# Optimization experiments

Hardware: AMD Instinct MI355X
Metric: run time of the kernel (lower is better)

Reference implementation:

```python
import jax, jax.numpy as jnp
from jax import lax
import numpy as np

DT = 0.02
STEP_JITTER = 0.01
NUM_STEPS = 180
B, H, W, D = 2, 512, 512, 128


def setup_inputs() -> dict:
    key = jax.random.key(0)
    k1, k2, k3 = jax.random.split(key, 3)
    camera_rotation = jnp.tile(jnp.eye(3, dtype=jnp.float32)[None], (B, 1, 1))
    camera_position = jnp.array([[0.0, 0.0, -2.5], [0.3, 0.2, -2.5]], dtype=jnp.float32)
    focal = 300.0 * jnp.ones((B, 2), dtype=jnp.float32)
    principal_point = jnp.full((B, 2), 256.0, dtype=jnp.float32)
    xs = jnp.arange(W, dtype=jnp.float32)
    ys = jnp.arange(H, dtype=jnp.float32)
    gx, gy = jnp.meshgrid(xs, ys, indexing='xy')  # [H,W]
    pixel_coords = jnp.broadcast_to(jnp.stack([gx, gy], -1)[None], (B, H, W, 2))
    template = jax.random.uniform(k1, (B, 4, D, D, D), dtype=jnp.float32)  # RGB + alpha volume
    background = jax.random.uniform(k2, (B, 3, H, W), dtype=jnp.float32)
    return {
        'camera_rotation': camera_rotation, 'camera_position': camera_position,
        'focal': focal, 'principal_point': principal_point,
        'pixel_coords': pixel_coords, 'template': template, 'background': background,
    }


def _trilinear_one(vol, pos):
    # vol [C,D,D,D] indexed [c,z,y,x]; pos [H,W,3] = (x,y,z) in [-1,1]
    Dv = vol.shape[-1]
    g = jnp.clip((pos + 1.0) * 0.5 * (Dv - 1), 0.0, Dv - 1)
    gx, gy, gz = g[..., 0], g[..., 1], g[..., 2]
    x0 = jnp.floor(gx).astype(jnp.int32); x1 = jnp.minimum(x0 + 1, Dv - 1)
    y0 = jnp.floor(gy).astype(jnp.int32); y1 = jnp.minimum(y0 + 1, Dv - 1)
    z0 = jnp.floor(gz).astype(jnp.int32); z1 = jnp.minimum(z0 + 1, Dv - 1)
    wx = (gx - x0)[None]; wy = (gy - y0)[None]; wz = (gz - z0)[None]
    at = lambda z, y, x: vol[:, z, y, x]  # [C,H,W]
    c00 = at(z0, y0, x0) * (1 - wx) + at(z0, y0, x1) * wx
    c01 = at(z0, y1, x0) * (1 - wx) + at(z0, y1, x1) * wx
    c10 = at(z1, y0, x0) * (1 - wx) + at(z1, y0, x1) * wx
    c11 = at(z1, y1, x0) * (1 - wx) + at(z1, y1, x1) * wx
    c0 = c00 * (1 - wy) + c01 * wy
    c1 = c10 * (1 - wy) + c11 * wy
    return c0 * (1 - wz) + c1 * wz  # [C,H,W]


def _march(camera_rotation, camera_position, focal, principal_point, pixel_coords, template, background):
    key = jax.random.key(42)
    rd = (pixel_coords - principal_point[:, None, None, :]) / focal[:, None, None, :]
    rd = jnp.concatenate([rd, jnp.ones_like(rd[..., :1])], axis=-1)
    # torch: sum(R[:,None,None,:,:] * d[...,:,None], dim=-2) == R^T @ d
    rd = jnp.einsum('bjk,bhwj->bhwk', camera_rotation, rd)
    rd = rd / jnp.sqrt(jnp.sum(rd * rd, axis=-1, keepdims=True))
    cp = camera_position[:, None, None, :]
    # ray/box intersection (no_grad in original)
    t1 = (-1.0 - cp) / rd
    t2 = (1.0 - cp) / rd
    t_min = jnp.maximum(jnp.minimum(t1[..., 0], t2[..., 0]),
                        jnp.maximum(jnp.minimum(t1[..., 1], t2[..., 1]),
                                    jnp.minimum(t1[..., 2], t2[..., 2])))
    t_max = jnp.minimum(jnp.maximum(t1[..., 0], t2[..., 0]),
                        jnp.minimum(jnp.maximum(t1[..., 1], t2[..., 1]),
                                    jnp.maximum(t1[..., 2], t2[..., 2])))
    hit = t_min < t_max
    t = jnp.maximum(jnp.where(hit, t_min, 0.0), 0.0)
    t = lax.stop_gradient(t)
    t = t - DT * jax.random.uniform(jax.random.fold_in(key, 0), t.shape, dtype=t.dtype)
    ray_pos = cp + rd * t[..., None]                      # [B,H,W,3]
    ray_rgb = jnp.zeros_like(jnp.moveaxis(ray_pos, -1, 1))  # [B,3,H,W]
    ray_alpha = jnp.zeros_like(ray_rgb[:, :1])             # [B,1,H,W]
    ray_length = jnp.zeros_like(ray_alpha)
    sample = jax.vmap(_trilinear_one)

    def body(carry, i):
        ray_pos, t, ray_rgb, ray_alpha, ray_length = carry
        valid = jnp.all((ray_pos > -1.0) & (ray_pos < 1.0), axis=-1)
        valid_f = valid[:, None].astype(ray_rgb.dtype)      # [B,1,H,W]
        s = sample(template, ray_pos)                       # [B,4,H,W]
        sample_rgb, sample_alpha = s[:, :3], s[:, 3:4]
        noise = jax.random.normal(jax.random.fold_in(key, i + 1), t.shape, dtype=t.dtype)
        step = lax.stop_gradient(DT * jnp.exp(STEP_JITTER * noise))  # [B,H,W]
        contrib = (jnp.minimum(ray_alpha + sample_alpha * step[:, None], 1.0) - ray_alpha) * valid_f
        ray_rgb = ray_rgb + sample_rgb * contrib
        ray_alpha = ray_alpha + contrib
        ray_length = ray_length + step[:, None] * (contrib == 0)
        ray_pos = ray_pos + rd * step[..., None]
        t = t + step
        return (ray_pos, t, ray_rgb, ray_alpha, ray_length), None

    carry = (ray_pos, t, ray_rgb, ray_alpha, ray_length)
    (ray_pos, t, ray_rgb, ray_alpha, ray_length), _ = lax.scan(body, carry, jnp.arange(NUM_STEPS))
    ray_length = ray_alpha * ray_length / (jnp.max(ray_length) + jnp.min(ray_length))
    ray_rgb = ray_rgb + (1.0 - ray_alpha) * jnp.maximum(background, 0.0)
    return ray_rgb, ray_alpha, ray_length


def reference(camera_rotation, camera_position, focal, principal_point, pixel_coords, template, background):
    return _march(camera_rotation, camera_position, focal, principal_point, pixel_coords, template, background)
```

## Files before the change

### kernel.cpp

```cpp
#include <hip/hip_runtime.h>
#include <stdint.h>

#pragma clang fp contract(off)

#define Bn 2
#define Hn 512
#define Wn 512
#define Dn 128
#define HW (Hn * Wn)
#define NRAY (Bn * HW)
#define NSTEP 180
#define DTC 0.02f
#define D3 (Dn * Dn * Dn)

#define WS_AOS_BYTE_OFF 4096
#define WS_AOS_BYTES ((size_t)Bn * D3 * 16)

typedef float f2 __attribute__((ext_vector_type(2)));

#define KEXP  ((float)(0.01 * (double)1.41421354f * 1.4426950408889634))
#define LOG2DT (-5.643856189774724f)

__device__ __forceinline__ uint32_t rotl32(uint32_t x, int n) {
    return (x << n) | (x >> (32 - n));
}

__device__ __forceinline__ void tf2x32(uint32_t k0, uint32_t k1,
                                       uint32_t& x0, uint32_t& x1) {
    uint32_t k2 = k0 ^ k1 ^ 0x1BD11BDAu;
    x0 += k0; x1 += k1;
    x0 += x1; x1 = rotl32(x1, 13); x1 ^= x0;
    x0 += x1; x1 = rotl32(x1, 15); x1 ^= x0;
    x0 += x1; x1 = rotl32(x1, 26); x1 ^= x0;
    x0 += x1; x1 = rotl32(x1, 6);  x1 ^= x0;
    x0 += k1; x1 += k2 + 1u;
    x0 += x1; x1 = rotl32(x1, 17); x1 ^= x0;
    x0 += x1; x1 = rotl32(x1, 29); x1 ^= x0;
    x0 += x1; x1 = rotl32(x1, 16); x1 ^= x0;
    x0 += x1; x1 = rotl32(x1, 24); x1 ^= x0;
    x0 += k2; x1 += k0 + 2u;
    x0 += x1; x1 = rotl32(x1, 13); x1 ^= x0;
    x0 += x1; x1 = rotl32(x1, 15); x1 ^= x0;
    x0 += x1; x1 = rotl32(x1, 26); x1 ^= x0;
    x0 += x1; x1 = rotl32(x1, 6);  x1 ^= x0;
    x0 += k0; x1 += k1 + 3u;
    x0 += x1; x1 = rotl32(x1, 17); x1 ^= x0;
    x0 += x1; x1 = rotl32(x1, 29); x1 ^= x0;
    x0 += x1; x1 = rotl32(x1, 16); x1 ^= x0;
    x0 += x1; x1 = rotl32(x1, 24); x1 ^= x0;
    x0 += k1; x1 += k2 + 4u;
    x0 += x1; x1 = rotl32(x1, 13); x1 ^= x0;
    x0 += x1; x1 = rotl32(x1, 15); x1 ^= x0;
    x0 += x1; x1 = rotl32(x1, 26); x1 ^= x0;
    x0 += x1; x1 = rotl32(x1, 6);  x1 ^= x0;
    x0 += k2; x1 += k0 + 5u;
}

__device__ __forceinline__ uint32_t pbits(uint32_t k0, uint32_t k1, uint32_t i) {
    uint32_t x0 = 0u, x1 = i;
    tf2x32(k0, k1, x0, x1);
    return x0 ^ x1;
}

__device__ __forceinline__ float erfinv_px(float x) {
    float a = x * x;
    float w = -__logf(1.0f - a);
    float p;
    if (w < 5.0f) {
        w = w - 2.5f;
        p = 2.81022636e-08f;
        p = fmaf(p, w, 3.43273939e-07f);
        p = fmaf(p, w, -3.5233877e-06f);
        p = fmaf(p, w, -4.39150654e-06f);
        p = fmaf(p, w, 0.00021858087f);
        p = fmaf(p, w, -0.00125372503f);
        p = fmaf(p, w, -0.00417768164f);
        p = fmaf(p, w, 0.246640727f);
        p = fmaf(p, w, 1.50140941f);
    } else {
        w = sqrtf(w) - 3.0f;
        p = -0.000200214257f;
        p = fmaf(p, w, 0.000100950558f);
        p = fmaf(p, w, 0.00134934322f);
        p = fmaf(p, w, -0.00367342844f);
        p = fmaf(p, w, 0.00573950773f);
        p = fmaf(p, w, -0.0076224613f);
        p = fmaf(p, w, 0.00943887047f);
        p = fmaf(p, w, 1.00167406f);
        p = fmaf(p, w, 2.83297682f);
    }
    return p * x;
}

__device__ __forceinline__ float step_from_bits(uint32_t bits) {
    float uf = __uint_as_float((bits >> 9) | 0x3f800000u);
    float uu = fmaxf(-0.99999994f, fmaf(uf, 2.0f, -3.0f));
    float pw = erfinv_px(uu);
    return __builtin_amdgcn_exp2f(fmaf(pw, KEXP, LOG2DT));
}

__device__ __forceinline__ f2 plerp(f2 a, f2 b, f2 wv) {
    return __builtin_elementwise_fma(wv, b - a, a);
}

__global__ void init_keys_kernel(uint32_t* __restrict__ ws) {
    int t = threadIdx.x;
    if (t <= 180) {
        uint32_t x0 = 0u, x1 = (uint32_t)t;
        tf2x32(0u, 42u, x0, x1);
        ws[2 * t]     = x0;
        ws[2 * t + 1] = x1;
    }
    if (t == 181) ws[362] = 0u;
    if (t == 182) ws[363] = 0x7f7fffffu;
}

__global__ __launch_bounds__(256) void repack_kernel(
    const float* __restrict__ tpl, float4* __restrict__ aos,
    uint32_t* __restrict__ ws) {
    if (blockIdx.x == 0) {
        int t = threadIdx.x;
        if (t <= 180) {
            uint32_t x0 = 0u, x1 = (uint32_t)t;
            tf2x32(0u, 42u, x0, x1);
            ws[2 * t]     = x0;
            ws[2 * t + 1] = x1;
        }
        if (t == 181) ws[362] = 0u;
        if (t == 182) ws[363] = 0x7f7fffffu;
    }
    int i = blockIdx.x * 256 + threadIdx.x;
    if (i >= Bn * D3) return;
    int b = i >> 21;
    int v = i & (D3 - 1);
    const float* base = tpl + (size_t)b * 4 * D3 + v;
    float4 o;
    o.x = base[0];
    o.y = base[D3];
    o.z = base[2 * D3];
    o.w = base[3 * D3];
    aos[i] = o;
}

template <bool PACKED>
__global__ __launch_bounds__(256) void march_kernel(
    const float* __restrict__ rot, const float* __restrict__ cpos,
    const float* __restrict__ focal, const float* __restrict__ pp,
    const float* __restrict__ pix, const float* __restrict__ tpl,
    const float4* __restrict__ aos,
    const float* __restrict__ bg, float* __restrict__ out,
    uint32_t* __restrict__ ws)
{
    #pragma clang fp contract(off)
    __shared__ uint2 skeys[181];
    for (int i = threadIdx.x; i < 181; i += 256) {
        skeys[i] = make_uint2(ws[2 * i], ws[2 * i + 1]);
    }
    __syncthreads();

    const int idx = blockIdx.x * 256 + threadIdx.x;
    const int b = idx >> 18;
    const int p = idx & (HW - 1);

    float px = pix[(size_t)idx * 2 + 0];
    float py = pix[(size_t)idx * 2 + 1];
    float v0 = (px - pp[b * 2 + 0]) / focal[b * 2 + 0];
    float v1 = (py - pp[b * 2 + 1]) / focal[b * 2 + 1];
    const float* R = rot + b * 9;
    float rdx = (R[0] * v0 + R[3] * v1) + R[6];
    float rdy = (R[1] * v0 + R[4] * v1) + R[7];
    float rdz = (R[2] * v0 + R[5] * v1) + R[8];
    float nrm = sqrtf((rdx * rdx + rdy * rdy) + rdz * rdz);
    rdx = rdx / nrm; rdy = rdy / nrm; rdz = rdz / nrm;
    float cpx = cpos[b * 3 + 0], cpy = cpos[b * 3 + 1], cpz = cpos[b * 3 + 2];

    float t1x = (-1.0f - cpx) / rdx, t2x = (1.0f - cpx) / rdx;
    float t1y = (-1.0f - cpy) / rdy, t2y = (1.0f - cpy) / rdy;
    float t1z = (-1.0f - cpz) / rdz, t2z = (1.0f - cpz) / rdz;
    float tmin = fmaxf(fminf(t1x, t2x), fmaxf(fminf(t1y, t2y), fminf(t1z, t2z)));
    float tmax = fminf(fmaxf(t1x, t2x), fminf(fmaxf(t1y, t2y), fmaxf(t1z, t2z)));
    bool hit = tmin < tmax;
    float t = fmaxf(hit ? tmin : 0.0f, 0.0f);

    {
        uint2 k0 = skeys[0];
        uint32_t bits = pbits(k0.x, k0.y, (uint32_t)idx);
        float u = __uint_as_float((bits >> 9) | 0x3f800000u) - 1.0f;
        u = fmaxf(0.0f, u);
        t = t - DTC * u;
    }

    float posx = cpx + rdx * t;
    float posy = cpy + rdy * t;
    float posz = cpz + rdz * t;

    float alpha = 0.0f, len = 0.0f;
    f2 acc_rg = {0.0f, 0.0f};
    float acc_b = 0.0f;
    const float* vol = tpl + (size_t)b * 4 * D3;
    const char* vbase = (const char*)(aos + (size_t)b * D3);
    bool entered = false;

    int i = 0;
    for (; i < NSTEP; ++i) {
        uint2 kk = skeys[i + 1];
        float step = step_from_bits(pbits(kk.x, kk.y, (uint32_t)idx));

        float m = fmaxf(fmaxf(fabsf(posx), fabsf(posy)), fabsf(posz));
        bool valid = m < 1.0f;
        bool sampling = fmaxf(m, alpha) < 1.0f;

        float contrib = 0.0f;
        if (sampling) {
            float gx = fmaf(posx, 63.5f, 63.5f);
            float gy = fmaf(posy, 63.5f, 63.5f);
            float gz = fmaf(posz, 63.5f, 63.5f);
            float fx = floorf(gx), fy = floorf(gy), fz = floorf(gz);
            float wx = gx - fx, wy = gy - fy, wz = gz - fz;
            int ix0 = (int)fx, iy0 = (int)fy, iz0 = (int)fz;

            float sx, sy, sz, sw;
            if (PACKED) {
                uint32_t xb  = (uint32_t)min(ix0, Dn - 2) << 4;
                float wxe = (ix0 < Dn - 1) ? wx : 1.0f;
                uint32_t yb0 = (uint32_t)iy0 << 11;
                uint32_t yb1 = min(yb0 + (1u << 11), (uint32_t)(Dn - 1) << 11);
                uint32_t zb0 = (uint32_t)iz0 << 18;
                uint32_t zb1 = min(zb0 + (1u << 18), (uint32_t)(Dn - 1) << 18);

                uint32_t o00 = zb0 + yb0 + xb;
                uint32_t o01 = zb0 + yb1 + xb;
                uint32_t o10 = zb1 + yb0 + xb;
                uint32_t o11 = zb1 + yb1 + xb;

                float4 A00 = *(const float4*)(vbase + o00);
                float4 B00 = *(const float4*)(vbase + o00 + 16);
                float4 A01 = *(const float4*)(vbase + o01);
                float4 B01 = *(const float4*)(vbase + o01 + 16);
                float4 A10 = *(const float4*)(vbase + o10);
                float4 B10 = *(const float4*)(vbase + o10 + 16);
                float4 A11 = *(const float4*)(vbase + o11);
                float4 B11 = *(const float4*)(vbase + o11 + 16);

                f2 wxv = {wxe, wxe}, wyv = {wy, wy}, wzv = {wz, wz};
                f2 c00rg = plerp((f2){A00.x, A00.y}, (f2){B00.x, B00.y}, wxv);
                f2 c00ba = plerp((f2){A00.z, A00.w}, (f2){B00.z, B00.w}, wxv);
                f2 c01rg = plerp((f2){A01.x, A01.y}, (f2){B01.x, B01.y}, wxv);
                f2 c01ba = plerp((f2){A01.z, A01.w}, (f2){B01.z, B01.w}, wxv);
                f2 c10rg = plerp((f2){A10.x, A10.y}, (f2){B10.x, B10.y}, wxv);
                f2 c10ba = plerp((f2){A10.z, A10.w}, (f2){B10.z, B10.w}, wxv);
                f2 c11rg = plerp((f2){A11.x, A11.y}, (f2){B11.x, B11.y}, wxv);
                f2 c11ba = plerp((f2){A11.z, A11.w}, (f2){B11.z, B11.w}, wxv);
                f2 c0rg = plerp(c00rg, c01rg, wyv);
                f2 c0ba = plerp(c00ba, c01ba, wyv);
                f2 c1rg = plerp(c10rg, c11rg, wyv);
                f2 c1ba = plerp(c10ba, c11ba, wyv);
                f2 srg = plerp(c0rg, c1rg, wzv);
                f2 sba = plerp(c0ba, c1ba, wzv);
                sx = srg.x; sy = srg.y; sz = sba.x; sw = sba.y;
            } else {
                int ix1 = min(ix0 + 1, Dn - 1);
                int iy1 = min(iy0 + 1, Dn - 1);
                int iz1 = min(iz0 + 1, Dn - 1);
                float owx = 1.0f - wx, owy = 1.0f - wy, owz = 1.0f - wz;
                size_t o00 = ((size_t)iz0 * Dn + iy0) * Dn;
                size_t o01 = ((size_t)iz0 * Dn + iy1) * Dn;
                size_t o10 = ((size_t)iz1 * Dn + iy0) * Dn;
                size_t o11 = ((size_t)iz1 * Dn + iy1) * Dn;
                float s[4];
                #pragma unroll
                for (int c = 0; c < 4; ++c) {
                    const float* vc = vol + (size_t)c * D3;
                    float c00 = vc[o00 + ix0] * owx + vc[o00 + ix1] * wx;
                    float c01 = vc[o01 + ix0] * owx + vc[o01 + ix1] * wx;
                    float c10 = vc[o10 + ix0] * owx + vc[o10 + ix1] * wx;
                    float c11 = vc[o11 + ix0] * owx + vc[o11 + ix1] * wx;
                    float cc0 = c00 * owy + c01 * wy;
                    float cc1 = c10 * owy + c11 * wy;
                    s[c] = cc0 * owz + cc1 * wz;
                }
                sx = s[0]; sy = s[1]; sz = s[2]; sw = s[3];
            }
            contrib = fminf(fmaf(sw, step, alpha), 1.0f) - alpha;
            f2 cv = {contrib, contrib};
            acc_rg = __builtin_elementwise_fma((f2){sx, sy}, cv, acc_rg);
            acc_b = fmaf(sz, contrib, acc_b);
        }
        alpha = alpha + contrib;
        if (contrib == 0.0f) len = len + step;
        posx = fmaf(rdx, step, posx);
        posy = fmaf(rdy, step, posy);
        posz = fmaf(rdz, step, posz);

        bool done = (alpha >= 1.0f) || (entered && !valid);
        entered = entered || valid;
        if (__all(done)) { ++i; break; }
    }
    for (; i < NSTEP; ++i) {
        uint2 kk = skeys[i + 1];
        len = len + step_from_bits(pbits(kk.x, kk.y, (uint32_t)idx));
    }

    size_t obase = (size_t)b * 3 * HW + p;
    out[obase]            = acc_rg.x + (1.0f - alpha) * fmaxf(bg[obase], 0.0f);
    out[obase + HW]       = acc_rg.y + (1.0f - alpha) * fmaxf(bg[obase + HW], 0.0f);
    out[obase + 2 * HW]   = acc_b   + (1.0f - alpha) * fmaxf(bg[obase + 2 * HW], 0.0f);
    out[(size_t)Bn * 3 * HW + (size_t)b * HW + p] = alpha;
    out[(size_t)Bn * 4 * HW + (size_t)b * HW + p] = len;

    __shared__ float smax[256];
    __shared__ float smin[256];
    smax[threadIdx.x] = len;
    smin[threadIdx.x] = len;
    __syncthreads();
    for (int s = 128; s > 0; s >>= 1) {
        if (threadIdx.x < s) {
            smax[threadIdx.x] = fmaxf(smax[threadIdx.x], smax[threadIdx.x + s]);
            smin[threadIdx.x] = fminf(smin[threadIdx.x], smin[threadIdx.x + s]);
        }
        __syncthreads();
    }
    if (threadIdx.x == 0) {
        atomicMax((unsigned int*)&ws[362], __float_as_uint(smax[0]));
        atomicMin((unsigned int*)&ws[363], __float_as_uint(smin[0]));
    }
}

__global__ void finalize_kernel(float* __restrict__ out,
                                const uint32_t* __restrict__ ws) {
    #pragma clang fp contract(off)
    int i = blockIdx.x * blockDim.x + threadIdx.x;
    if (i >= NRAY) return;
    float mx = __uint_as_float(ws[362]);
    float mn = __uint_as_float(ws[363]);
    float a = out[(size_t)Bn * 3 * HW + i];
    size_t loff = (size_t)Bn * 4 * HW + i;
    float l = out[loff];
    out[loff] = (a * l) / (mx + mn);
}

extern "C" void kernel_launch(void* const* d_in, const int* in_sizes, int n_in,
                              void* d_out, int out_size, void* d_ws, size_t ws_size,
                              hipStream_t stream) {
    const float* rot   = (const float*)d_in[0];
    const float* cpos  = (const float*)d_in[1];
    const float* focal = (const float*)d_in[2];
    const float* pp    = (const float*)d_in[3];
    const float* pix   = (const float*)d_in[4];
    const float* tpl   = (const float*)d_in[5];
    const float* bg    = (const float*)d_in[6];
    float* out = (float*)d_out;
    uint32_t* ws = (uint32_t*)d_ws;
    float4* aos = (float4*)((char*)d_ws + WS_AOS_BYTE_OFF);

    const bool packed = ws_size >= WS_AOS_BYTE_OFF + WS_AOS_BYTES;

    if (packed) {
        hipLaunchKernelGGL(repack_kernel, dim3((Bn * D3) / 256), dim3(256), 0,
                           stream, tpl, aos, ws);
        hipLaunchKernelGGL(march_kernel<true>, dim3(NRAY / 256), dim3(256), 0,
                           stream, rot, cpos, focal, pp, pix, tpl, aos, bg, out, ws);
    } else {
        hipLaunchKernelGGL(init_keys_kernel, dim3(1), dim3(256), 0, stream, ws);
        hipLaunchKernelGGL(march_kernel<false>, dim3(NRAY / 256), dim3(256), 0,
                           stream, rot, cpos, focal, pp, pix, tpl, aos, bg, out, ws);
    }
    hipLaunchKernelGGL(finalize_kernel, dim3(NRAY / 256), dim3(256), 0, stream,
                       out, ws);
}
```

Baseline: 434.7 us.

## March two rays per thread with interleaved Threefry and per-ray wave masks

```diff
diff --git a/kernel.cpp b/kernel.cpp
--- a/kernel.cpp
+++ b/kernel.cpp
@@ -56,13 +56,36 @@
     x0 += k2; x1 += k0 + 5u;
 }
 
-__device__ __forceinline__ uint32_t pbits(uint32_t k0, uint32_t k1, uint32_t i) {
-    uint32_t x0 = 0u, x1 = i;
-    tf2x32(k0, k1, x0, x1);
-    return x0 ^ x1;
+__device__ __forceinline__ void tf2x32_pair(uint32_t k0, uint32_t k1,
+                                            uint32_t& a0, uint32_t& a1,
+                                            uint32_t& b0, uint32_t& b1) {
+    uint32_t k2 = k0 ^ k1 ^ 0x1BD11BDAu;
+#define QR(x0, x1, r) x0 += x1; x1 = rotl32(x1, r); x1 ^= x0;
+#define QR2(r) QR(a0, a1, r) QR(b0, b1, r)
+    a0 += k0; a1 += k1;          b0 += k0; b1 += k1;
+    QR2(13) QR2(15) QR2(26) QR2(6)
+    a0 += k1; a1 += k2 + 1u;     b0 += k1; b1 += k2 + 1u;
+    QR2(17) QR2(29) QR2(16) QR2(24)
+    a0 += k2; a1 += k0 + 2u;     b0 += k2; b1 += k0 + 2u;
+    QR2(13) QR2(15) QR2(26) QR2(6)
+    a0 += k0; a1 += k1 + 3u;     b0 += k0; b1 += k1 + 3u;
+    QR2(17) QR2(29) QR2(16) QR2(24)
+    a0 += k1; a1 += k2 + 4u;     b0 += k1; b1 += k2 + 4u;
+    QR2(13) QR2(15) QR2(26) QR2(6)
+    a0 += k2; a1 += k0 + 5u;     b0 += k2; b1 += k0 + 5u;
+#undef QR2
+#undef QR
+}
+
+__device__ __forceinline__ uint2 pbits2(uint32_t k0, uint32_t k1,
+                                        uint32_t ia, uint32_t ib) {
+    uint32_t a0 = 0u, a1 = ia, b0 = 0u, b1 = ib;
+    tf2x32_pair(k0, k1, a0, a1, b0, b1);
+    return make_uint2(a0 ^ a1, b0 ^ b1);
 }
 
 __device__ __forceinline__ float erfinv_px(float x) {
+    #pragma clang fp contract(off)
     float a = x * x;
     float w = -__logf(1.0f - a);
     float p;
@@ -93,6 +116,7 @@
 }
 
 __device__ __forceinline__ float step_from_bits(uint32_t bits) {
+    #pragma clang fp contract(off)
     float uf = __uint_as_float((bits >> 9) | 0x3f800000u);
     float uu = fmaxf(-0.99999994f, fmaf(uf, 2.0f, -3.0f));
     float pw = erfinv_px(uu);
@@ -142,26 +166,21 @@
     aos[i] = o;
 }
 
-template <bool PACKED>
-__global__ __launch_bounds__(256) void march_kernel(
+struct Ray {
+    float rdx, rdy, rdz;
+    float posx, posy, posz;
+    float alpha, len;
+    f2 acc_rg;
+    float acc_b;
+    bool entered;
+    bool done;
+};
+
+__device__ __forceinline__ void ray_setup(int idx, int b,
     const float* __restrict__ rot, const float* __restrict__ cpos,
     const float* __restrict__ focal, const float* __restrict__ pp,
-    const float* __restrict__ pix, const float* __restrict__ tpl,
-    const float4* __restrict__ aos,
-    const float* __restrict__ bg, float* __restrict__ out,
-    uint32_t* __restrict__ ws)
-{
-    #pragma clang fp contract(off)
-    __shared__ uint2 skeys[181];
-    for (int i = threadIdx.x; i < 181; i += 256) {
-        skeys[i] = make_uint2(ws[2 * i], ws[2 * i + 1]);
-    }
-    __syncthreads();
-
-    const int idx = blockIdx.x * 256 + threadIdx.x;
-    const int b = idx >> 18;
-    const int p = idx & (HW - 1);
-
+    const float* __restrict__ pix, uint32_t jbits, Ray& r) {
+    #pragma clang fp contract(off)
     float px = pix[(size_t)idx * 2 + 0];
     float py = pix[(size_t)idx * 2 + 1];
     float v0 = (px - pp[b * 2 + 0]) / focal[b * 2 + 0];
@@ -182,136 +201,191 @@
     bool hit = tmin < tmax;
     float t = fmaxf(hit ? tmin : 0.0f, 0.0f);
 
+    float u = __uint_as_float((jbits >> 9) | 0x3f800000u) - 1.0f;
+    u = fmaxf(0.0f, u);
+    t = t - DTC * u;
+
+    r.rdx = rdx; r.rdy = rdy; r.rdz = rdz;
+    r.posx = cpx + rdx * t;
+    r.posy = cpy + rdy * t;
+    r.posz = cpz + rdz * t;
+    r.alpha = 0.0f; r.len = 0.0f;
+    r.acc_rg = (f2){0.0f, 0.0f};
+    r.acc_b = 0.0f;
+    r.entered = false;
+    r.done = !hit;
+}
+
+template <bool PACKED>
+__device__ __forceinline__ void march_step(Ray& r, float step,
+    const char* __restrict__ vbase, const float* __restrict__ vol) {
+    #pragma clang fp contract(off)
+    float m = fmaxf(fmaxf(fabsf(r.posx), fabsf(r.posy)), fabsf(r.posz));
+    bool valid = m < 1.0f;
+    bool sampling = fmaxf(m, r.alpha) < 1.0f;
+
+    float contrib = 0.0f;
+    if (sampling) {
+        float gx = fmaf(r.posx, 63.5f, 63.5f);
+        float gy = fmaf(r.posy, 63.5f, 63.5f);
+        float gz = fmaf(r.posz, 63.5f, 63.5f);
+        float fx = floorf(gx), fy = floorf(gy), fz = floorf(gz);
+        float wx = gx - fx, wy = gy - fy, wz = gz - fz;
+        int ix0 = (int)fx, iy0 = (int)fy, iz0 = (int)fz;
+
+        float sx, sy, sz, sw;
+        if (PACKED) {
+            uint32_t xb  = (uint32_t)min(ix0, Dn - 2) << 4;
+            float wxe = (ix0 < Dn - 1) ? wx : 1.0f;
+            uint32_t yb0 = (uint32_t)iy0 << 11;
+            uint32_t yb1 = min(yb0 + (1u << 11), (uint32_t)(Dn - 1) << 11);
+            uint32_t zb0 = (uint32_t)iz0 << 18;
+            uint32_t zb1 = min(zb0 + (1u << 18), (uint32_t)(Dn - 1) << 18);
+
+            uint32_t o00 = zb0 + yb0 + xb;
+            uint32_t o01 = zb0 + yb1 + xb;
+            uint32_t o10 = zb1 + yb0 + xb;
+            uint32_t o11 = zb1 + yb1 + xb;
+
+            float4 A00 = *(const float4*)(vbase + o00);
+            float4 B00 = *(const float4*)(vbase + o00 + 16);
+            float4 A01 = *(const float4*)(vbase + o01);
+            float4 B01 = *(const float4*)(vbase + o01 + 16);
+            float4 A10 = *(const float4*)(vbase + o10);
+            float4 B10 = *(const float4*)(vbase + o10 + 16);
+            float4 A11 = *(const float4*)(vbase + o11);
+            float4 B11 = *(const float4*)(vbase + o11 + 16);
+
+            f2 wxv = {wxe, wxe}, wyv = {wy, wy}, wzv = {wz, wz};
+            f2 c00rg = plerp((f2){A00.x, A00.y}, (f2){B00.x, B00.y}, wxv);
+            f2 c00ba = plerp((f2){A00.z, A00.w}, (f2){B00.z, B00.w}, wxv);
+            f2 c01rg = plerp((f2){A01.x, A01.y}, (f2){B01.x, B01.y}, wxv);
+            f2 c01ba = plerp((f2){A01.z, A01.w}, (f2){B01.z, B01.w}, wxv);
+            f2 c10rg = plerp((f2){A10.x, A10.y}, (f2){B10.x, B10.y}, wxv);
+            f2 c10ba = plerp((f2){A10.z, A10.w}, (f2){B10.z, B10.w}, wxv);
+            f2 c11rg = plerp((f2){A11.x, A11.y}, (f2){B11.x, B11.y}, wxv);
+            f2 c11ba = plerp((f2){A11.z, A11.w}, (f2){B11.z, B11.w}, wxv);
+            f2 c0rg = plerp(c00rg, c01rg, wyv);
+            f2 c0ba = plerp(c00ba, c01ba, wyv);
+            f2 c1rg = plerp(c10rg, c11rg, wyv);
+            f2 c1ba = plerp(c10ba, c11ba, wyv);
+            f2 srg = plerp(c0rg, c1rg, wzv);
+            f2 sba = plerp(c0ba, c1ba, wzv);
+            sx = srg.x; sy = srg.y; sz = sba.x; sw = sba.y;
+        } else {
+            int ix1 = min(ix0 + 1, Dn - 1);
+            int iy1 = min(iy0 + 1, Dn - 1);
+            int iz1 = min(iz0 + 1, Dn - 1);
+            float owx = 1.0f - wx, owy = 1.0f - wy, owz = 1.0f - wz;
+            size_t o00 = ((size_t)iz0 * Dn + iy0) * Dn;
+            size_t o01 = ((size_t)iz0 * Dn + iy1) * Dn;
+            size_t o10 = ((size_t)iz1 * Dn + iy0) * Dn;
+            size_t o11 = ((size_t)iz1 * Dn + iy1) * Dn;
+            float s[4];
+            #pragma unroll
+            for (int c = 0; c < 4; ++c) {
+                const float* vc = vol + (size_t)c * D3;
+                float c00 = vc[o00 + ix0] * owx + vc[o00 + ix1] * wx;
+                float c01 = vc[o01 + ix0] * owx + vc[o01 + ix1] * wx;
+                float c10 = vc[o10 + ix0] * owx + vc[o10 + ix1] * wx;
+                float c11 = vc[o11 + ix0] * owx + vc[o11 + ix1] * wx;
+                float cc0 = c00 * owy + c01 * wy;
+                float cc1 = c10 * owy + c11 * wy;
+                s[c] = cc0 * owz + cc1 * wz;
+            }
+            sx = s[0]; sy = s[1]; sz = s[2]; sw = s[3];
+        }
+        contrib = fminf(fmaf(sw, step, r.alpha), 1.0f) - r.alpha;
+        f2 cv = {contrib, contrib};
+        r.acc_rg = __builtin_elementwise_fma((f2){sx, sy}, cv, r.acc_rg);
+        r.acc_b = fmaf(sz, contrib, r.acc_b);
+    }
+    r.alpha = r.alpha + contrib;
+    if (contrib == 0.0f) r.len = r.len + step;
+    r.posx = fmaf(r.rdx, step, r.posx);
+    r.posy = fmaf(r.rdy, step, r.posy);
+    r.posz = fmaf(r.rdz, step, r.posz);
+
+    bool done_now = (r.alpha >= 1.0f) || (r.entered && !valid);
+    r.entered = r.entered || valid;
+    r.done = r.done || done_now;
+}
+
+__device__ __forceinline__ void write_ray(float* __restrict__ out,
+    const float* __restrict__ bg, int b, int p, const Ray& r) {
+    #pragma clang fp contract(off)
+    size_t obase = (size_t)b * 3 * HW + p;
+    out[obase]          = r.acc_rg.x + (1.0f - r.alpha) * fmaxf(bg[obase], 0.0f);
+    out[obase + HW]     = r.acc_rg.y + (1.0f - r.alpha) * fmaxf(bg[obase + HW], 0.0f);
+    out[obase + 2 * HW] = r.acc_b   + (1.0f - r.alpha) * fmaxf(bg[obase + 2 * HW], 0.0f);
+    out[(size_t)Bn * 3 * HW + (size_t)b * HW + p] = r.alpha;
+    out[(size_t)Bn * 4 * HW + (size_t)b * HW + p] = r.len;
+}
+
+template <bool PACKED>
+__global__ __launch_bounds__(256, 4) void march2_kernel(
+    const float* __restrict__ rot, const float* __restrict__ cpos,
+    const float* __restrict__ focal, const float* __restrict__ pp,
+    const float* __restrict__ pix, const float* __restrict__ tpl,
+    const float4* __restrict__ aos,
+    const float* __restrict__ bg, float* __restrict__ out,
+    uint32_t* __restrict__ ws)
+{
+    #pragma clang fp contract(off)
+    __shared__ uint2 skeys[181];
+    for (int i = threadIdx.x; i < 181; i += 256) {
+        skeys[i] = make_uint2(ws[2 * i], ws[2 * i + 1]);
+    }
+    __syncthreads();
+
+    const int g = blockIdx.x * 256 + threadIdx.x;
+    const int b = g >> 17;
+    const int pA = g & 0x1FFFF;
+    const int pB = pA + 0x20000;
+    const int idxA = (b << 18) + pA;
+    const int idxB = idxA + 0x20000;
+
+    Ray ra, rb;
     {
         uint2 k0 = skeys[0];
-        uint32_t bits = pbits(k0.x, k0.y, (uint32_t)idx);
-        float u = __uint_as_float((bits >> 9) | 0x3f800000u) - 1.0f;
-        u = fmaxf(0.0f, u);
-        t = t - DTC * u;
-    }
-
-    float posx = cpx + rdx * t;
-    float posy = cpy + rdy * t;
-    float posz = cpz + rdz * t;
-
-    float alpha = 0.0f, len = 0.0f;
-    f2 acc_rg = {0.0f, 0.0f};
-    float acc_b = 0.0f;
+        uint2 jb = pbits2(k0.x, k0.y, (uint32_t)idxA, (uint32_t)idxB);
+        ray_setup(idxA, b, rot, cpos, focal, pp, pix, jb.x, ra);
+        ray_setup(idxB, b, rot, cpos, focal, pp, pix, jb.y, rb);
+    }
+
     const float* vol = tpl + (size_t)b * 4 * D3;
     const char* vbase = (const char*)(aos + (size_t)b * D3);
-    bool entered = false;
-
-    int i = 0;
-    for (; i < NSTEP; ++i) {
+
+    bool mA = !__all(ra.done);
+    bool mB = !__all(rb.done);
+
+    for (int i = 0; i < NSTEP; ++i) {
         uint2 kk = skeys[i + 1];
-        float step = step_from_bits(pbits(kk.x, kk.y, (uint32_t)idx));
-
-        float m = fmaxf(fmaxf(fabsf(posx), fabsf(posy)), fabsf(posz));
-        bool valid = m < 1.0f;
-        bool sampling = fmaxf(m, alpha) < 1.0f;
-
-        float contrib = 0.0f;
-        if (sampling) {
-            float gx = fmaf(posx, 63.5f, 63.5f);
-            float gy = fmaf(posy, 63.5f, 63.5f);
-            float gz = fmaf(posz, 63.5f, 63.5f);
-            float fx = floorf(gx), fy = floorf(gy), fz = floorf(gz);
-            float wx = gx - fx, wy = gy - fy, wz = gz - fz;
-            int ix0 = (int)fx, iy0 = (int)fy, iz0 = (int)fz;
-
-            float sx, sy, sz, sw;
-            if (PACKED) {
-                uint32_t xb  = (uint32_t)min(ix0, Dn - 2) << 4;
-                float wxe = (ix0 < Dn - 1) ? wx : 1.0f;
-                uint32_t yb0 = (uint32_t)iy0 << 11;
-                uint32_t yb1 = min(yb0 + (1u << 11), (uint32_t)(Dn - 1) << 11);
-                uint32_t zb0 = (uint32_t)iz0 << 18;
-                uint32_t zb1 = min(zb0 + (1u << 18), (uint32_t)(Dn - 1) << 18);
-
-                uint32_t o00 = zb0 + yb0 + xb;
-                uint32_t o01 = zb0 + yb1 + xb;
-                uint32_t o10 = zb1 + yb0 + xb;
-                uint32_t o11 = zb1 + yb1 + xb;
-
-                float4 A00 = *(const float4*)(vbase + o00);
-                float4 B00 = *(const float4*)(vbase + o00 + 16);
-                float4 A01 = *(const float4*)(vbase + o01);
-                float4 B01 = *(const float4*)(vbase + o01 + 16);
-                float4 A10 = *(const float4*)(vbase + o10);
-                float4 B10 = *(const float4*)(vbase + o10 + 16);
-                float4 A11 = *(const float4*)(vbase + o11);
-                float4 B11 = *(const float4*)(vbase + o11 + 16);
-
-                f2 wxv = {wxe, wxe}, wyv = {wy, wy}, wzv = {wz, wz};
-                f2 c00rg = plerp((f2){A00.x, A00.y}, (f2){B00.x, B00.y}, wxv);
-                f2 c00ba = plerp((f2){A00.z, A00.w}, (f2){B00.z, B00.w}, wxv);
-                f2 c01rg = plerp((f2){A01.x, A01.y}, (f2){B01.x, B01.y}, wxv);
-                f2 c01ba = plerp((f2){A01.z, A01.w}, (f2){B01.z, B01.w}, wxv);
-                f2 c10rg = plerp((f2){A10.x, A10.y}, (f2){B10.x, B10.y}, wxv);
-                f2 c10ba = plerp((f2){A10.z, A10.w}, (f2){B10.z, B10.w}, wxv);
-                f2 c11rg = plerp((f2){A11.x, A11.y}, (f2){B11.x, B11.y}, wxv);
-                f2 c11ba = plerp((f2){A11.z, A11.w}, (f2){B11.z, B11.w}, wxv);
-                f2 c0rg = plerp(c00rg, c01rg, wyv);
-                f2 c0ba = plerp(c00ba, c01ba, wyv);
-                f2 c1rg = plerp(c10rg, c11rg, wyv);
-                f2 c1ba = plerp(c10ba, c11ba, wyv);
-                f2 srg = plerp(c0rg, c1rg, wzv);
-                f2 sba = plerp(c0ba, c1ba, wzv);
-                sx = srg.x; sy = srg.y; sz = sba.x; sw = sba.y;
-            } else {
-                int ix1 = min(ix0 + 1, Dn - 1);
-                int iy1 = min(iy0 + 1, Dn - 1);
-                int iz1 = min(iz0 + 1, Dn - 1);
-                float owx = 1.0f - wx, owy = 1.0f - wy, owz = 1.0f - wz;
-                size_t o00 = ((size_t)iz0 * Dn + iy0) * Dn;
-                size_t o01 = ((size_t)iz0 * Dn + iy1) * Dn;
-                size_t o10 = ((size_t)iz1 * Dn + iy0) * Dn;
-                size_t o11 = ((size_t)iz1 * Dn + iy1) * Dn;
-                float s[4];
-                #pragma unroll
-                for (int c = 0; c < 4; ++c) {
-                    const float* vc = vol + (size_t)c * D3;
-                    float c00 = vc[o00 + ix0] * owx + vc[o00 + ix1] * wx;
-                    float c01 = vc[o01 + ix0] * owx + vc[o01 + ix1] * wx;
-                    float c10 = vc[o10 + ix0] * owx + vc[o10 + ix1] * wx;
-                    float c11 = vc[o11 + ix0] * owx + vc[o11 + ix1] * wx;
-                    float cc0 = c00 * owy + c01 * wy;
-                    float cc1 = c10 * owy + c11 * wy;
-                    s[c] = cc0 * owz + cc1 * wz;
-                }
-                sx = s[0]; sy = s[1]; sz = s[2]; sw = s[3];
-            }
-            contrib = fminf(fmaf(sw, step, alpha), 1.0f) - alpha;
-            f2 cv = {contrib, contrib};
-            acc_rg = __builtin_elementwise_fma((f2){sx, sy}, cv, acc_rg);
-            acc_b = fmaf(sz, contrib, acc_b);
+        uint2 bits = pbits2(kk.x, kk.y, (uint32_t)idxA, (uint32_t)idxB);
+        float stepA = step_from_bits(bits.x);
+        float stepB = step_from_bits(bits.y);
+
+        if (mA) {
+            march_step<PACKED>(ra, stepA, vbase, vol);
+            mA = !__all(ra.done);
+        } else {
+            ra.len = ra.len + stepA;
         }
-        alpha = alpha + contrib;
-        if (contrib == 0.0f) len = len + step;
-        posx = fmaf(rdx, step, posx);
-        posy = fmaf(rdy, step, posy);
-        posz = fmaf(rdz, step, posz);
-
-        bool done = (alpha >= 1.0f) || (entered && !valid);
-        entered = entered || valid;
-        if (__all(done)) { ++i; break; }
-    }
-    for (; i < NSTEP; ++i) {
-        uint2 kk = skeys[i + 1];
-        len = len + step_from_bits(pbits(kk.x, kk.y, (uint32_t)idx));
-    }
-
-    size_t obase = (size_t)b * 3 * HW + p;
-    out[obase]            = acc_rg.x + (1.0f - alpha) * fmaxf(bg[obase], 0.0f);
-    out[obase + HW]       = acc_rg.y + (1.0f - alpha) * fmaxf(bg[obase + HW], 0.0f);
-    out[obase + 2 * HW]   = acc_b   + (1.0f - alpha) * fmaxf(bg[obase + 2 * HW], 0.0f);
-    out[(size_t)Bn * 3 * HW + (size_t)b * HW + p] = alpha;
-    out[(size_t)Bn * 4 * HW + (size_t)b * HW + p] = len;
+        if (mB) {
+            march_step<PACKED>(rb, stepB, vbase, vol);
+            mB = !__all(rb.done);
+        } else {
+            rb.len = rb.len + stepB;
+        }
+    }
+
+    write_ray(out, bg, b, pA, ra);
+    write_ray(out, bg, b, pB, rb);
 
     __shared__ float smax[256];
     __shared__ float smin[256];
-    smax[threadIdx.x] = len;
-    smin[threadIdx.x] = len;
+    smax[threadIdx.x] = fmaxf(ra.len, rb.len);
+    smin[threadIdx.x] = fminf(ra.len, rb.len);
     __syncthreads();
     for (int s = 128; s > 0; s >>= 1) {
         if (threadIdx.x < s) {
@@ -358,11 +432,11 @@
     if (packed) {
         hipLaunchKernelGGL(repack_kernel, dim3((Bn * D3) / 256), dim3(256), 0,
                            stream, tpl, aos, ws);
-        hipLaunchKernelGGL(march_kernel<true>, dim3(NRAY / 256), dim3(256), 0,
+        hipLaunchKernelGGL(march2_kernel<true>, dim3(NRAY / 512), dim3(256), 0,
                            stream, rot, cpos, focal, pp, pix, tpl, aos, bg, out, ws);
     } else {
         hipLaunchKernelGGL(init_keys_kernel, dim3(1), dim3(256), 0, stream, ws);
-        hipLaunchKernelGGL(march_kernel<false>, dim3(NRAY / 256), dim3(256), 0,
+        hipLaunchKernelGGL(march2_kernel<false>, dim3(NRAY / 512), dim3(256), 0,
                            stream, rot, cpos, focal, pp, pix, tpl, aos, bg, out, ws);
     }
     hipLaunchKernelGGL(finalize_kernel, dim3(NRAY / 256), dim3(256), 0, stream,
```

After: 445.4 us. 1.02x slower.

## Software-pipeline volume gathers and RNG one step ahead in ray march loop

Applied to the files above, without the earlier changes.

```diff
diff --git a/kernel.cpp b/kernel.cpp
--- a/kernel.cpp
+++ b/kernel.cpp
@@ -56,6 +56,29 @@
     x0 += k2; x1 += k0 + 5u;
 }
 
+__device__ __forceinline__ void tf2x32_pk(uint32_t ka0, uint32_t ka1,
+                                          uint32_t kb0, uint32_t kb1,
+                                          uint32_t& a0, uint32_t& a1,
+                                          uint32_t& b0, uint32_t& b1) {
+    uint32_t ka2 = ka0 ^ ka1 ^ 0x1BD11BDAu;
+    uint32_t kb2 = kb0 ^ kb1 ^ 0x1BD11BDAu;
+#define QR(x0, x1, r) x0 += x1; x1 = rotl32(x1, r); x1 ^= x0;
+#define QR2(r) QR(a0, a1, r) QR(b0, b1, r)
+    a0 += ka0; a1 += ka1;          b0 += kb0; b1 += kb1;
+    QR2(13) QR2(15) QR2(26) QR2(6)
+    a0 += ka1; a1 += ka2 + 1u;     b0 += kb1; b1 += kb2 + 1u;
+    QR2(17) QR2(29) QR2(16) QR2(24)
+    a0 += ka2; a1 += ka0 + 2u;     b0 += kb2; b1 += kb0 + 2u;
+    QR2(13) QR2(15) QR2(26) QR2(6)
+    a0 += ka0; a1 += ka1 + 3u;     b0 += kb0; b1 += kb1 + 3u;
+    QR2(17) QR2(29) QR2(16) QR2(24)
+    a0 += ka1; a1 += ka2 + 4u;     b0 += kb1; b1 += kb2 + 4u;
+    QR2(13) QR2(15) QR2(26) QR2(6)
+    a0 += ka2; a1 += ka0 + 5u;     b0 += kb2; b1 += kb0 + 5u;
+#undef QR2
+#undef QR
+}
+
 __device__ __forceinline__ uint32_t pbits(uint32_t k0, uint32_t k1, uint32_t i) {
     uint32_t x0 = 0u, x1 = i;
     tf2x32(k0, k1, x0, x1);
@@ -63,6 +86,7 @@
 }
 
 __device__ __forceinline__ float erfinv_px(float x) {
+    #pragma clang fp contract(off)
     float a = x * x;
     float w = -__logf(1.0f - a);
     float p;
@@ -93,6 +117,7 @@
 }
 
 __device__ __forceinline__ float step_from_bits(uint32_t bits) {
+    #pragma clang fp contract(off)
     float uf = __uint_as_float((bits >> 9) | 0x3f800000u);
     float uu = fmaxf(-0.99999994f, fmaf(uf, 2.0f, -3.0f));
     float pw = erfinv_px(uu);
@@ -142,8 +167,43 @@
     aos[i] = o;
 }
 
+__device__ __forceinline__ void issue_loads(const char* __restrict__ vbase,
+    float posx, float posy, float posz,
+    float4 (&L)[8], float& wxe, float& wy, float& wz) {
+    #pragma clang fp contract(off)
+    float gx = fmaf(posx, 63.5f, 63.5f);
+    float gy = fmaf(posy, 63.5f, 63.5f);
+    float gz = fmaf(posz, 63.5f, 63.5f);
+    float fx = floorf(gx), fy = floorf(gy), fz = floorf(gz);
+    float wx = gx - fx;
+    wy = gy - fy;
+    wz = gz - fz;
+    int ix0 = (int)fx, iy0 = (int)fy, iz0 = (int)fz;
+    int ixc = min(max(ix0, 0), Dn - 2);
+    int iyc = min(max(iy0, 0), Dn - 1);
+    int izc = min(max(iz0, 0), Dn - 1);
+    wxe = (ix0 < Dn - 1) ? wx : 1.0f;
+    uint32_t xb  = (uint32_t)ixc << 4;
+    uint32_t yb0 = (uint32_t)iyc << 11;
+    uint32_t yb1 = min(yb0 + (1u << 11), (uint32_t)(Dn - 1) << 11);
+    uint32_t zb0 = (uint32_t)izc << 18;
+    uint32_t zb1 = min(zb0 + (1u << 18), (uint32_t)(Dn - 1) << 18);
+    uint32_t o00 = zb0 + yb0 + xb;
+    uint32_t o01 = zb0 + yb1 + xb;
+    uint32_t o10 = zb1 + yb0 + xb;
+    uint32_t o11 = zb1 + yb1 + xb;
+    L[0] = *(const float4*)(vbase + o00);
+    L[1] = *(const float4*)(vbase + o00 + 16);
+    L[2] = *(const float4*)(vbase + o01);
+    L[3] = *(const float4*)(vbase + o01 + 16);
+    L[4] = *(const float4*)(vbase + o10);
+    L[5] = *(const float4*)(vbase + o10 + 16);
+    L[6] = *(const float4*)(vbase + o11);
+    L[7] = *(const float4*)(vbase + o11 + 16);
+}
+
 template <bool PACKED>
-__global__ __launch_bounds__(256) void march_kernel(
+__global__ __launch_bounds__(256, 4) void march_kernel(
     const float* __restrict__ rot, const float* __restrict__ cpos,
     const float* __restrict__ focal, const float* __restrict__ pp,
     const float* __restrict__ pix, const float* __restrict__ tpl,
@@ -197,104 +257,132 @@
     float alpha = 0.0f, len = 0.0f;
     f2 acc_rg = {0.0f, 0.0f};
     float acc_b = 0.0f;
-    const float* vol = tpl + (size_t)b * 4 * D3;
-    const char* vbase = (const char*)(aos + (size_t)b * D3);
     bool entered = false;
+    bool done = !hit;
 
     int i = 0;
-    for (; i < NSTEP; ++i) {
-        uint2 kk = skeys[i + 1];
-        float step = step_from_bits(pbits(kk.x, kk.y, (uint32_t)idx));
-
-        float m = fmaxf(fmaxf(fabsf(posx), fabsf(posy)), fabsf(posz));
-        bool valid = m < 1.0f;
-        bool sampling = fmaxf(m, alpha) < 1.0f;
-
-        float contrib = 0.0f;
-        if (sampling) {
-            float gx = fmaf(posx, 63.5f, 63.5f);
-            float gy = fmaf(posy, 63.5f, 63.5f);
-            float gz = fmaf(posz, 63.5f, 63.5f);
-            float fx = floorf(gx), fy = floorf(gy), fz = floorf(gz);
-            float wx = gx - fx, wy = gy - fy, wz = gz - fz;
-            int ix0 = (int)fx, iy0 = (int)fy, iz0 = (int)fz;
-
-            float sx, sy, sz, sw;
-            if (PACKED) {
-                uint32_t xb  = (uint32_t)min(ix0, Dn - 2) << 4;
-                float wxe = (ix0 < Dn - 1) ? wx : 1.0f;
-                uint32_t yb0 = (uint32_t)iy0 << 11;
-                uint32_t yb1 = min(yb0 + (1u << 11), (uint32_t)(Dn - 1) << 11);
-                uint32_t zb0 = (uint32_t)iz0 << 18;
-                uint32_t zb1 = min(zb0 + (1u << 18), (uint32_t)(Dn - 1) << 18);
-
-                uint32_t o00 = zb0 + yb0 + xb;
-                uint32_t o01 = zb0 + yb1 + xb;
-                uint32_t o10 = zb1 + yb0 + xb;
-                uint32_t o11 = zb1 + yb1 + xb;
-
-                float4 A00 = *(const float4*)(vbase + o00);
-                float4 B00 = *(const float4*)(vbase + o00 + 16);
-                float4 A01 = *(const float4*)(vbase + o01);
-                float4 B01 = *(const float4*)(vbase + o01 + 16);
-                float4 A10 = *(const float4*)(vbase + o10);
-                float4 B10 = *(const float4*)(vbase + o10 + 16);
-                float4 A11 = *(const float4*)(vbase + o11);
-                float4 B11 = *(const float4*)(vbase + o11 + 16);
-
-                f2 wxv = {wxe, wxe}, wyv = {wy, wy}, wzv = {wz, wz};
-                f2 c00rg = plerp((f2){A00.x, A00.y}, (f2){B00.x, B00.y}, wxv);
-                f2 c00ba = plerp((f2){A00.z, A00.w}, (f2){B00.z, B00.w}, wxv);
-                f2 c01rg = plerp((f2){A01.x, A01.y}, (f2){B01.x, B01.y}, wxv);
-                f2 c01ba = plerp((f2){A01.z, A01.w}, (f2){B01.z, B01.w}, wxv);
-                f2 c10rg = plerp((f2){A10.x, A10.y}, (f2){B10.x, B10.y}, wxv);
-                f2 c10ba = plerp((f2){A10.z, A10.w}, (f2){B10.z, B10.w}, wxv);
-                f2 c11rg = plerp((f2){A11.x, A11.y}, (f2){B11.x, B11.y}, wxv);
-                f2 c11ba = plerp((f2){A11.z, A11.w}, (f2){B11.z, B11.w}, wxv);
-                f2 c0rg = plerp(c00rg, c01rg, wyv);
-                f2 c0ba = plerp(c00ba, c01ba, wyv);
-                f2 c1rg = plerp(c10rg, c11rg, wyv);
-                f2 c1ba = plerp(c10ba, c11ba, wyv);
-                f2 srg = plerp(c0rg, c1rg, wzv);
-                f2 sba = plerp(c0ba, c1ba, wzv);
-                sx = srg.x; sy = srg.y; sz = sba.x; sw = sba.y;
-            } else {
-                int ix1 = min(ix0 + 1, Dn - 1);
-                int iy1 = min(iy0 + 1, Dn - 1);
-                int iz1 = min(iz0 + 1, Dn - 1);
-                float owx = 1.0f - wx, owy = 1.0f - wy, owz = 1.0f - wz;
-                size_t o00 = ((size_t)iz0 * Dn + iy0) * Dn;
-                size_t o01 = ((size_t)iz0 * Dn + iy1) * Dn;
-                size_t o10 = ((size_t)iz1 * Dn + iy0) * Dn;
-                size_t o11 = ((size_t)iz1 * Dn + iy1) * Dn;
-                float s[4];
-                #pragma unroll
-                for (int c = 0; c < 4; ++c) {
-                    const float* vc = vol + (size_t)c * D3;
-                    float c00 = vc[o00 + ix0] * owx + vc[o00 + ix1] * wx;
-                    float c01 = vc[o01 + ix0] * owx + vc[o01 + ix1] * wx;
-                    float c10 = vc[o10 + ix0] * owx + vc[o10 + ix1] * wx;
-                    float c11 = vc[o11 + ix0] * owx + vc[o11 + ix1] * wx;
-                    float cc0 = c00 * owy + c01 * wy;
-                    float cc1 = c10 * owy + c11 * wy;
-                    s[c] = cc0 * owz + cc1 * wz;
+    if constexpr (PACKED) {
+        const char* vbase = (const char*)(aos + (size_t)b * D3);
+        if (!__all(done)) {
+            float m = fmaxf(fmaxf(fabsf(posx), fabsf(posy)), fabsf(posz));
+            bool valid = m < 1.0f;
+            bool samp  = m < 1.0f;
+            float4 L[8];
+            float wxe = 0.0f, wy = 0.0f, wz = 0.0f;
+            if (__any(samp)) issue_loads(vbase, posx, posy, posz, L, wxe, wy, wz);
+            uint2 k1 = skeys[1];
+            float s_cur = step_from_bits(pbits(k1.x, k1.y, (uint32_t)idx));
+
+            for (; i < NSTEP; ++i) {
+                uint2 kn = skeys[min(i + 2, 180)];
+                uint32_t bnext = pbits(kn.x, kn.y, (uint32_t)idx);
+
+                float contrib = 0.0f;
+                if (samp) {
+                    f2 wxv = {wxe, wxe}, wyv = {wy, wy}, wzv = {wz, wz};
+                    f2 c00rg = plerp((f2){L[0].x, L[0].y}, (f2){L[1].x, L[1].y}, wxv);
+                    f2 c00ba = plerp((f2){L[0].z, L[0].w}, (f2){L[1].z, L[1].w}, wxv);
+                    f2 c01rg = plerp((f2){L[2].x, L[2].y}, (f2){L[3].x, L[3].y}, wxv);
+                    f2 c01ba = plerp((f2){L[2].z, L[2].w}, (f2){L[3].z, L[3].w}, wxv);
+                    f2 c10rg = plerp((f2){L[4].x, L[4].y}, (f2){L[5].x, L[5].y}, wxv);
+                    f2 c10ba = plerp((f2){L[4].z, L[4].w}, (f2){L[5].z, L[5].w}, wxv);
+                    f2 c11rg = plerp((f2){L[6].x, L[6].y}, (f2){L[7].x, L[7].y}, wxv);
+                    f2 c11ba = plerp((f2){L[6].z, L[6].w}, (f2){L[7].z, L[7].w}, wxv);
+                    f2 c0rg = plerp(c00rg, c01rg, wyv);
+                    f2 c0ba = plerp(c00ba, c01ba, wyv);
+                    f2 c1rg = plerp(c10rg, c11rg, wyv);
+                    f2 c1ba = plerp(c10ba, c11ba, wyv);
+                    f2 srg = plerp(c0rg, c1rg, wzv);
+                    f2 sba = plerp(c0ba, c1ba, wzv);
+                    contrib = fminf(fmaf(sba.y, s_cur, alpha), 1.0f) - alpha;
+                    f2 cv = {contrib, contrib};
+                    acc_rg = __builtin_elementwise_fma(srg, cv, acc_rg);
+                    acc_b = fmaf(sba.x, contrib, acc_b);
                 }
-                sx = s[0]; sy = s[1]; sz = s[2]; sw = s[3];
+                alpha = alpha + contrib;
+                if (contrib == 0.0f) len = len + s_cur;
+                posx = fmaf(rdx, s_cur, posx);
+                posy = fmaf(rdy, s_cur, posy);
+                posz = fmaf(rdz, s_cur, posz);
+
+                bool done_now = (alpha >= 1.0f) || (entered && !valid);
+                entered = entered || valid;
+                done = done || done_now;
+
+                float m2 = fmaxf(fmaxf(fabsf(posx), fabsf(posy)), fabsf(posz));
+                valid = m2 < 1.0f;
+                bool samp_n = fmaxf(m2, alpha) < 1.0f;
+                float s_nx = step_from_bits(bnext);
+                if (__any(samp_n)) issue_loads(vbase, posx, posy, posz, L, wxe, wy, wz);
+                samp = samp_n;
+                s_cur = s_nx;
+
+                if (__all(done)) { ++i; break; }
             }
-            contrib = fminf(fmaf(sw, step, alpha), 1.0f) - alpha;
-            f2 cv = {contrib, contrib};
-            acc_rg = __builtin_elementwise_fma((f2){sx, sy}, cv, acc_rg);
-            acc_b = fmaf(sz, contrib, acc_b);
         }
-        alpha = alpha + contrib;
-        if (contrib == 0.0f) len = len + step;
-        posx = fmaf(rdx, step, posx);
-        posy = fmaf(rdy, step, posy);
-        posz = fmaf(rdz, step, posz);
-
-        bool done = (alpha >= 1.0f) || (entered && !valid);
-        entered = entered || valid;
-        if (__all(done)) { ++i; break; }
+    } else {
+        const float* vol = tpl + (size_t)b * 4 * D3;
+        if (!__all(done)) {
+            for (; i < NSTEP; ++i) {
+                uint2 kk = skeys[i + 1];
+                float step = step_from_bits(pbits(kk.x, kk.y, (uint32_t)idx));
+                float m = fmaxf(fmaxf(fabsf(posx), fabsf(posy)), fabsf(posz));
+                bool valid = m < 1.0f;
+                bool sampling = fmaxf(m, alpha) < 1.0f;
+                float contrib = 0.0f;
+                if (sampling) {
+                    float gx = fmaf(posx, 63.5f, 63.5f);
+                    float gy = fmaf(posy, 63.5f, 63.5f);
+                    float gz = fmaf(posz, 63.5f, 63.5f);
+                    float fx = floorf(gx), fy = floorf(gy), fz = floorf(gz);
+                    float wx = gx - fx, wy = gy - fy, wz = gz - fz;
+                    int ix0 = (int)fx, iy0 = (int)fy, iz0 = (int)fz;
+                    int ix1 = min(ix0 + 1, Dn - 1);
+                    int iy1 = min(iy0 + 1, Dn - 1);
+                    int iz1 = min(iz0 + 1, Dn - 1);
+                    float owx = 1.0f - wx, owy = 1.0f - wy, owz = 1.0f - wz;
+                    size_t o00 = ((size_t)iz0 * Dn + iy0) * Dn;
+                    size_t o01 = ((size_t)iz0 * Dn + iy1) * Dn;
+                    size_t o10 = ((size_t)iz1 * Dn + iy0) * Dn;
+                    size_t o11 = ((size_t)iz1 * Dn + iy1) * Dn;
+                    float s[4];
+                    #pragma unroll
+                    for (int c = 0; c < 4; ++c) {
+                        const float* vc = vol + (size_t)c * D3;
+                        float c00 = vc[o00 + ix0] * owx + vc[o00 + ix1] * wx;
+                        float c01 = vc[o01 + ix0] * owx + vc[o01 + ix1] * wx;
+                        float c10 = vc[o10 + ix0] * owx + vc[o10 + ix1] * wx;
+                        float c11 = vc[o11 + ix0] * owx + vc[o11 + ix1] * wx;
+                        float cc0 = c00 * owy + c01 * wy;
+                        float cc1 = c10 * owy + c11 * wy;
+                        s[c] = cc0 * owz + cc1 * wz;
+                    }
+                    contrib = fminf(fmaf(s[3], step, alpha), 1.0f) - alpha;
+                    f2 cv = {contrib, contrib};
+                    acc_rg = __builtin_elementwise_fma((f2){s[0], s[1]}, cv, acc_rg);
+                    acc_b = fmaf(s[2], contrib, acc_b);
+                }
+                alpha = alpha + contrib;
+                if (contrib == 0.0f) len = len + step;
+                posx = fmaf(rdx, step, posx);
+                posy = fmaf(rdy, step, posy);
+                posz = fmaf(rdz, step, posz);
+                bool done_now = (alpha >= 1.0f) || (entered && !valid);
+                entered = entered || valid;
+                done = done || done_now;
+                if (__all(done)) { ++i; break; }
+            }
+        }
+    }
+
+    for (; i + 1 < NSTEP; i += 2) {
+        uint2 kA = skeys[i + 1];
+        uint2 kB = skeys[i + 2];
+        uint32_t a0 = 0u, a1 = (uint32_t)idx;
+        uint32_t c0 = 0u, c1 = (uint32_t)idx;
+        tf2x32_pk(kA.x, kA.y, kB.x, kB.y, a0, a1, c0, c1);
+        len = len + step_from_bits(a0 ^ a1);
+        len = len + step_from_bits(c0 ^ c1);
     }
     for (; i < NSTEP; ++i) {
         uint2 kk = skeys[i + 1];
```

Result: faster. 421.5 us (-3.0%).
